# Kernel optimization log

Measured on AMD Instinct MI355X. Metric: run time of the kernel, lower is better.

## Reference

```python
import jax, jax.numpy as jnp
import numpy as np

B_SZ, SEQ, D_MODEL, D_STATE, KSIZE = 8, 4096, 1024, 64, 64
DT_MIN, DT_MAX = 0.001, 0.1


def setup_inputs() -> dict:
    key = jax.random.key(0)
    k1, k2, k3, k4 = jax.random.split(key, 4)
    u = jax.random.normal(k1, (B_SZ, SEQ, D_MODEL), dtype=jnp.float32)
    # HiPPO-like init: A = -(n+1)
    A = -(jnp.arange(D_STATE, dtype=jnp.float32) + 1.0)
    Bp = 0.01 * jax.random.normal(k2, (D_STATE, D_MODEL), dtype=jnp.float32)
    Cp = 0.01 * jax.random.normal(k3, (D_MODEL, D_STATE), dtype=jnp.float32)
    Dp = jnp.ones((D_MODEL,), dtype=jnp.float32)
    log_dt = jnp.log(jax.random.uniform(k4, (D_MODEL,), dtype=jnp.float32,
                                        minval=DT_MIN, maxval=DT_MAX))
    return {"u": u, "A": A, "B": Bp, "C": Cp, "D": Dp, "log_dt": log_dt}


def reference(u, A, B, C, D, log_dt):
    # u: (batch, seq_len, d_model)
    batch, seq_len, d_model = u.shape
    L = min(seq_len, KSIZE)  # truncated SSM kernel length

    # --- SSM kernel (same math as ssm_kernel) ---
    dt = jnp.exp(log_dt)                         # (d_model,)
    A_bar = jnp.exp(A[:, None] * dt[None, :])    # (d_state, d_model)
    powers = jnp.arange(L)[:, None, None]        # (L,1,1)
    A_powers = A_bar[None, :, :] ** powers       # (L, d_state, d_model)
    # K[l,k] = sum_{m,d} C[m,d] * A_bar[d,k]^l * B[d,k]  (faithful to original einsum)
    K = jnp.einsum('md,ldk,dk->lk', C, A_powers, B)  # (L, d_model)

    # --- Batched per-channel 'same' convolution via FFT ---
    # Equivalent to jnp.convolve(u[b,:,i], K[:,i], mode='same') for every b, i,
    # with L <= seq_len so the 'same' slice starts at (L-1)//2.
    n = seq_len + L - 1
    Uf = jnp.fft.rfft(u, n=n, axis=1)            # (batch, nf, d_model)
    Kf = jnp.fft.rfft(K, n=n, axis=0)            # (nf, d_model)
    conv_full = jnp.fft.irfft(Uf * Kf[None], n=n, axis=1)  # (batch, n, d_model)
    start = (L - 1) // 2
    y = conv_full[:, start:start + seq_len, :]

    # skip connection
    y = y + D[None, None, :] * u
    return y
```

## Files before the change

kernel.cpp:

```cpp
#include <hip/hip_runtime.h>

#define SEQ 4096
#define DM 1024
#define DS 64
#define KS 64

#define TCH 64
#define TT  128
#define R   16

__global__ void csum_kernel(const float* __restrict__ C, float* __restrict__ csum) {
    int d    = threadIdx.x & 63;
    int mloc = threadIdx.x >> 6;
    int m0   = blockIdx.x * 64;
    float s = 0.f;
#pragma unroll
    for (int j = 0; j < 16; ++j)
        s += C[(m0 + j * 4 + mloc) * DS + d];
    __shared__ float red[4][64];
    red[mloc][d] = s;
    __syncthreads();
    if (threadIdx.x < 64) {
        float t = red[0][d] + red[1][d] + red[2][d] + red[3][d];
        atomicAdd(&csum[d], t);
    }
}

__global__ void taps_kernel(const float* __restrict__ A, const float* __restrict__ B,
                            const float* __restrict__ log_dt,
                            const float* __restrict__ csum, float* __restrict__ Ktl) {
    int g = blockIdx.x * blockDim.x + threadIdx.x;
    int k = g & (DM - 1);
    int l = g >> 10;
    float dt = __expf(log_dt[k]);
    float fl = (float)l;
    float acc = 0.f;
#pragma unroll 8
    for (int d = 0; d < DS; ++d)
        acc += csum[d] * __expf(A[d] * dt * fl) * B[d * DM + k];
    Ktl[g] = acc;
}

template<bool GUARD>
__device__ __forceinline__ float2 ldu(const float2* __restrict__ up2, int t) {
    if (GUARD) {
        if (t >= 0 && t < SEQ) return up2[(size_t)t * (DM / 2)];
        return make_float2(0.f, 0.f);
    }
    return up2[(size_t)t * (DM / 2)];
}

template<bool GUARD>
__device__ __forceinline__ void do_tile(const float2* __restrict__ up2,
                                        float2* __restrict__ yp2,
                                        const float (*tapsL)[66],
                                        float2 D2, int ts, int c2) {
    float2 acc[R];
#pragma unroll
    for (int r = 0; r < R; ++r) acc[r] = make_float2(0.f, 0.f);

    float2 w[31];
#pragma unroll
    for (int i = 0; i < 31; ++i) w[i] = ldu<GUARD>(up2, ts + 16 + i);

#pragma unroll
    for (int c = 0; c < 4; ++c) {
        if (c > 0) {
#pragma unroll
            for (int i = 30; i >= 16; --i) w[i] = w[i - 16];
            int wb = ts + 16 - 16 * c;
#pragma unroll
            for (int i = 0; i < 16; ++i) w[i] = ldu<GUARD>(up2, wb + i);
        }
        if (c == 1) {
#pragma unroll
            for (int r = 0; r < R; ++r) {
                acc[r].x = fmaf(D2.x, w[r].x, acc[r].x);
                acc[r].y = fmaf(D2.y, w[r].y, acc[r].y);
            }
        }
#pragma unroll
        for (int j = 0; j < 16; ++j) {
            float2 t2 = *(const float2*)&tapsL[16 * c + j][2 * c2];
#pragma unroll
            for (int r = 0; r < R; ++r) {
                acc[r].x = fmaf(t2.x, w[r + 15 - j].x, acc[r].x);
                acc[r].y = fmaf(t2.y, w[r + 15 - j].y, acc[r].y);
            }
        }
    }

#pragma unroll
    for (int r = 0; r < R; ++r)
        yp2[(size_t)(ts + r) * (DM / 2)] = acc[r];
}

__global__ __launch_bounds__(256)
void conv_kernel(const float* __restrict__ u, const float* __restrict__ Ktl,
                 const float* __restrict__ D, float* __restrict__ y) {
    __shared__ __align__(16) float tapsL[KS][66];

    int k0 = blockIdx.x * TCH;
    int t0 = blockIdx.y * TT;
    int b  = blockIdx.z;

    for (int i = threadIdx.x; i < KS * TCH; i += 256) {
        int l = i >> 6, kk = i & 63;
        tapsL[l][kk] = Ktl[l * DM + k0 + kk];
    }
    __syncthreads();

    int c2 = threadIdx.x & 31;
    int tg = threadIdx.x >> 5;
    int ts = t0 + tg * R;
    int p  = (k0 >> 1) + c2;

    const float2* up2 = (const float2*)u + (size_t)b * SEQ * (DM / 2) + p;
    float2*       yp2 = (float2*)y       + (size_t)b * SEQ * (DM / 2) + p;
    float2 D2 = *(const float2*)(D + k0 + 2 * c2);

    bool interior = (t0 >= 32) && (t0 + 159 <= SEQ);
    if (interior) do_tile<false>(up2, yp2, tapsL, D2, ts, c2);
    else          do_tile<true >(up2, yp2, tapsL, D2, ts, c2);
}

extern "C" void kernel_launch(void* const* d_in, const int* in_sizes, int n_in,
                              void* d_out, int out_size, void* d_ws, size_t ws_size,
                              hipStream_t stream) {
    const float* u      = (const float*)d_in[0];
    const float* A      = (const float*)d_in[1];
    const float* Bp     = (const float*)d_in[2];
    const float* Cp     = (const float*)d_in[3];
    const float* Dp     = (const float*)d_in[4];
    const float* log_dt = (const float*)d_in[5];
    float* y = (float*)d_out;

    float* csum = (float*)d_ws;
    float* Ktl  = csum + 64;

    hipMemsetAsync(csum, 0, DS * sizeof(float), stream);
    csum_kernel<<<16, 256, 0, stream>>>(Cp, csum);
    taps_kernel<<<(DM * KS) / 256, 256, 0, stream>>>(A, Bp, log_dt, csum, Ktl);

    dim3 grid(DM / TCH, SEQ / TT, 8);
    conv_kernel<<<grid, 256, 0, stream>>>(u, Ktl, Dp, y);
}
```

Before: 312.6 us.

## Stage input halo tile and taps into LDS via async global_load_lds

The conv kernel now copies the whole 192-row by 64-channel input tile (with halo) and the tap table into shared memory using the global_load_lds builtin, instead of each thread loading its sliding window straight from global memory. Edge tiles use ordinary zero-padded float4 loads into LDS. The goal is to cut redundant global and L2 traffic from overlapping windows and to issue wide, coalesced copies. In exchange it uses about 64KB of LDS per block, which limits occupancy, and adds a full barrier before compute.

```diff
diff --git a/kernel.cpp b/kernel.cpp
--- a/kernel.cpp
+++ b/kernel.cpp
@@ -8,6 +8,13 @@
 #define TCH 64
 #define TT  128
 #define R   16
+#define NROW (TT + 64)
+
+typedef const __attribute__((address_space(1))) void* gas_ptr;
+typedef __attribute__((address_space(3))) void* las_ptr;
+__device__ __forceinline__ void async_cp16(const void* g, void* s) {
+    __builtin_amdgcn_global_load_lds((gas_ptr)g, (las_ptr)s, 16, 0, 0);
+}
 
 __global__ void csum_kernel(const float* __restrict__ C, float* __restrict__ csum) {
     int d    = threadIdx.x & 63;
@@ -41,36 +48,81 @@
     Ktl[g] = acc;
 }
 
-template<bool GUARD>
-__device__ __forceinline__ float2 ldu(const float2* __restrict__ up2, int t) {
-    if (GUARD) {
-        if (t >= 0 && t < SEQ) return up2[(size_t)t * (DM / 2)];
-        return make_float2(0.f, 0.f);
+__global__ __launch_bounds__(256, 2)
+void conv_kernel(const float* __restrict__ u, const float* __restrict__ Ktl,
+                 const float* __restrict__ D, float* __restrict__ y) {
+    __shared__ __align__(16) float smem_u[NROW * TCH];
+    __shared__ __align__(16) float smem_t[KS * TCH];
+
+    int k0 = blockIdx.x * TCH;
+    int t0 = blockIdx.y * TT;
+    int b  = blockIdx.z;
+
+    int lane = threadIdx.x & 63;
+    int wv   = threadIdx.x >> 6;
+
+    const float* gt = u + (size_t)b * SEQ * DM + (size_t)(t0 - 32) * DM + k0;
+
+    bool interior = (blockIdx.y > 0) && (blockIdx.y + 1 < SEQ / TT);
+
+#pragma unroll
+    for (int j = 0; j < 4; ++j) {
+        int fb = j * 4096 + wv * 1024;
+        int f  = fb + lane * 16;
+        int l  = f >> 8;
+        int c  = (f & 255) >> 2;
+        async_cp16(Ktl + l * DM + k0 + c, (char*)smem_t + fb);
     }
-    return up2[(size_t)t * (DM / 2)];
-}
 
-template<bool GUARD>
-__device__ __forceinline__ void do_tile(const float2* __restrict__ up2,
-                                        float2* __restrict__ yp2,
-                                        const float (*tapsL)[66],
-                                        float2 D2, int ts, int c2) {
+    if (interior) {
+#pragma unroll
+        for (int j = 0; j < 12; ++j) {
+            int fb = j * 4096 + wv * 1024;
+            int f  = fb + lane * 16;
+            int r  = f >> 8;
+            int c  = (f & 255) >> 2;
+            async_cp16(gt + (size_t)r * DM + c, (char*)smem_u + fb);
+        }
+    } else {
+#pragma unroll
+        for (int j = 0; j < 12; ++j) {
+            int f = j * 4096 + threadIdx.x * 16;
+            int r = f >> 8;
+            int c = (f & 255) >> 2;
+            int t = t0 - 32 + r;
+            float4 v = make_float4(0.f, 0.f, 0.f, 0.f);
+            if (t >= 0 && t < SEQ)
+                v = *(const float4*)(gt + (size_t)r * DM + c);
+            *(float4*)((char*)smem_u + f) = v;
+        }
+    }
+    __syncthreads();
+
+    int c2 = threadIdx.x & 31;
+    int tg = threadIdx.x >> 5;
+    int ts = t0 + tg * R;
+    int rb = tg * R;
+
+    const float2* us = (const float2*)smem_u;
+    const float2* tp = (const float2*)smem_t;
+
     float2 acc[R];
 #pragma unroll
     for (int r = 0; r < R; ++r) acc[r] = make_float2(0.f, 0.f);
 
     float2 w[31];
 #pragma unroll
-    for (int i = 0; i < 31; ++i) w[i] = ldu<GUARD>(up2, ts + 16 + i);
+    for (int i = 0; i < 31; ++i) w[i] = us[(rb + 48 + i) * 32 + c2];
+
+    float2 D2 = *(const float2*)(D + k0 + 2 * c2);
 
 #pragma unroll
     for (int c = 0; c < 4; ++c) {
         if (c > 0) {
 #pragma unroll
             for (int i = 30; i >= 16; --i) w[i] = w[i - 16];
-            int wb = ts + 16 - 16 * c;
 #pragma unroll
-            for (int i = 0; i < 16; ++i) w[i] = ldu<GUARD>(up2, wb + i);
+            for (int i = 0; i < 16; ++i) w[i] = us[(rb + 48 - 16 * c + i) * 32 + c2];
         }
         if (c == 1) {
 #pragma unroll
@@ -81,7 +133,7 @@
         }
 #pragma unroll
         for (int j = 0; j < 16; ++j) {
-            float2 t2 = *(const float2*)&tapsL[16 * c + j][2 * c2];
+            float2 t2 = tp[(16 * c + j) * 32 + c2];
 #pragma unroll
             for (int r = 0; r < R; ++r) {
                 acc[r].x = fmaf(t2.x, w[r + 15 - j].x, acc[r].x);
@@ -90,38 +142,10 @@
         }
     }
 
+    float2* yp2 = (float2*)y + (size_t)b * SEQ * (DM / 2) + (size_t)ts * (DM / 2) + (k0 >> 1) + c2;
 #pragma unroll
     for (int r = 0; r < R; ++r)
-        yp2[(size_t)(ts + r) * (DM / 2)] = acc[r];
-}
-
-__global__ __launch_bounds__(256)
-void conv_kernel(const float* __restrict__ u, const float* __restrict__ Ktl,
-                 const float* __restrict__ D, float* __restrict__ y) {
-    __shared__ __align__(16) float tapsL[KS][66];
-
-    int k0 = blockIdx.x * TCH;
-    int t0 = blockIdx.y * TT;
-    int b  = blockIdx.z;
-
-    for (int i = threadIdx.x; i < KS * TCH; i += 256) {
-        int l = i >> 6, kk = i & 63;
-        tapsL[l][kk] = Ktl[l * DM + k0 + kk];
-    }
-    __syncthreads();
-
-    int c2 = threadIdx.x & 31;
-    int tg = threadIdx.x >> 5;
-    int ts = t0 + tg * R;
-    int p  = (k0 >> 1) + c2;
-
-    const float2* up2 = (const float2*)u + (size_t)b * SEQ * (DM / 2) + p;
-    float2*       yp2 = (float2*)y       + (size_t)b * SEQ * (DM / 2) + p;
-    float2 D2 = *(const float2*)(D + k0 + 2 * c2);
-
-    bool interior = (t0 >= 32) && (t0 + 159 <= SEQ);
-    if (interior) do_tile<false>(up2, yp2, tapsL, D2, ts, c2);
-    else          do_tile<true >(up2, yp2, tapsL, D2, ts, c2);
+        yp2[(size_t)r * (DM / 2)] = acc[r];
 }
 
 extern "C" void kernel_launch(void* const* d_in, const int* in_sizes, int n_in,
```

New measurement: 269.8 us. 13.7% less time.
